# Performance work log

Measured on AMD Instinct MI355X. Metric: run time of the kernel, lower is better.

The kernel has to match this reference:

```python
import jax, jax.numpy as jnp
import numpy as np

NUM_CLASSES = 20
IOU_T = 0.5
NEG_RATIO = 3.0
VXY = 0.1
VWH = 0.2
EPS16 = 9.765625e-4  # torch.finfo(torch.float16).eps


def ltrb2xywh(b):
    return jnp.concatenate([(b[..., :2] + b[..., 2:]) * 0.5, b[..., 2:] - b[..., :2]], -1)


def xywh2ltrb(b):
    return jnp.concatenate([b[..., :2] - b[..., 2:] * 0.5, b[..., :2] + b[..., 2:] * 0.5], -1)


def pairwise_iou(gb, ab):
    # gb [G,4] ltrb, ab [A,4] ltrb -> [G,A]
    lt = jnp.maximum(gb[:, None, :2], ab[None, :, :2])
    rb = jnp.minimum(gb[:, None, 2:], ab[None, :, 2:])
    wh = jnp.clip(rb - lt, 0.0)
    inter = wh[..., 0] * wh[..., 1]
    area_g = (gb[:, 2] - gb[:, 0]) * (gb[:, 3] - gb[:, 1])
    area_a = (ab[:, 2] - ab[:, 0]) * (ab[:, 3] - ab[:, 1])
    return inter / jnp.clip(area_g[:, None] + area_a[None, :] - inter, 1e-8)


def setup_inputs() -> dict:
    key = jax.random.key(0)
    k = jax.random.split(key, 7)
    B, A, G, C = 64, 8732, 50, NUM_CLASSES + 1
    preg = jax.random.normal(k[0], (B, 4, A), jnp.float32) * 0.1
    pcls = jax.random.normal(k[1], (B, C, A), jnp.float32)
    acxy = jax.random.uniform(k[2], (A, 2), jnp.float32)
    awh = jax.random.uniform(k[3], (A, 2), jnp.float32, 0.05, 0.5)
    ancs_xywh = jnp.concatenate([acxy, awh], -1)
    gcxy = jax.random.uniform(k[4], (B, G, 2), jnp.float32, 0.2, 0.8)
    gwh = jax.random.uniform(k[5], (B, G, 2), jnp.float32, 0.05, 0.4)
    gboxes_ltrb = jnp.concatenate([gcxy - gwh * 0.5, gcxy + gwh * 0.5], -1)
    glabels = jax.random.randint(k[6], (B, G), 0, C)  # 0 == padding/background
    return {"preg": preg, "pcls": pcls, "ancs_xywh": ancs_xywh,
            "gboxes_ltrb": gboxes_ltrb, "glabels": glabels}


def _loss(preg, pcls, ancs_xywh, gboxes_ltrb, glabels):
    B, _, A = preg.shape
    preg_bad = jnp.transpose(preg, (0, 2, 1))  # [B,A,4]
    anc_ltrb = xywh2ltrb(ancs_xywh)

    def match(gb, gl):
        iou = pairwise_iou(gb, anc_ltrb)                    # [G,A]
        iou = jnp.where((gl > 0)[:, None], iou, -1.0)       # mask padded gts
        return jnp.argmax(iou, 0), jnp.max(iou, 0) >= IOU_T  # best gt per anchor, pos mask

    boxes_index, mask_pos = jax.vmap(match)(gboxes_ltrb, glabels)  # [B,A],[B,A]

    glabel = jnp.where(mask_pos, jnp.take_along_axis(glabels, boxes_index, 1), 0)  # [B,A]
    gbox_ltrb = jnp.take_along_axis(gboxes_ltrb, boxes_index[..., None], 1)        # [B,A,4]

    gxywh = ltrb2xywh(gbox_ltrb)
    txy = (gxywh[..., :2] - ancs_xywh[None, :, :2]) / (ancs_xywh[None, :, 2:] * VXY)
    twh = jnp.log(jnp.clip(gxywh[..., 2:], 1e-6) / ancs_xywh[None, :, 2:]) / VWH
    gtxywh = jnp.concatenate([txy, twh], -1)
    d = preg_bad - gtxywh
    ad = jnp.abs(d)
    sl1 = jnp.where(ad < 1.0, 0.5 * d * d, ad - 0.5).sum(-1)   # [B,A]
    posf = mask_pos.astype(preg.dtype)
    n_pos_total = jnp.clip(posf.sum(), 1.0)
    l_box = (sl1 * posf).sum() / n_pos_total

    # ---- classification: CE + OHEM hard negatives ----
    logp = jax.nn.log_softmax(pcls, axis=1)                     # [B,C,A]
    ce = -jnp.take_along_axis(logp, glabel[:, None, :], 1)[:, 0, :]  # [B,A]
    nums_pos = jnp.clip(posf.sum(-1), EPS16)                    # [B]

    loss_neg = jnp.where(mask_pos, 0.0, ce)
    order = jnp.argsort(-loss_neg, axis=-1)
    rank = jnp.argsort(order, axis=-1)
    mask_neg = (rank < (NEG_RATIO * nums_pos)[:, None]) & (~mask_pos)
    negf = mask_neg.astype(preg.dtype)

    l_conf_pos = ((ce * posf).sum(-1) / nums_pos).mean()
    l_conf_neg = ((ce * negf).sum(-1) / nums_pos).mean()
    return l_box + l_conf_pos + l_conf_neg


def reference(preg, pcls, ancs_xywh, gboxes_ltrb, glabels):
    return _loss(preg, pcls, ancs_xywh, gboxes_ltrb, glabels)
```

## Files before the change

kernel.cpp:

```cpp
#include <hip/hip_runtime.h>

#define B_ 64
#define A_ 8732
#define G_ 50
#define C_ 21
#define NBA 9
#define NBB 18
#define NV 35

__global__ __launch_bounds__(256) void k_match(
    const float* __restrict__ preg,
    const float* __restrict__ ancs,
    const float* __restrict__ gbox,
    const int*   __restrict__ glab,
    unsigned char* __restrict__ lab_out,
    int*   __restrict__ pos_part,
    float* __restrict__ sl1_part)
{
    __shared__ float4 sg[G_];
    __shared__ float  sa[G_];
    __shared__ int    slb[G_];
    __shared__ float  redf[4];
    __shared__ int    redi[4];
    const int b = blockIdx.y, tid = threadIdx.x;
    const int wid = tid >> 6, lane = tid & 63;
    int a0 = blockIdx.x * 1024 + tid * 4;
    const bool valid = a0 < A_;
    if (!valid) a0 = A_ - 4;

    if (tid < G_) {
        float4 gp = ((const float4*)gbox)[b * G_ + tid];
        const int lb = glab[b * G_ + tid];
        slb[tid] = lb;
        if (lb <= 0) gp = make_float4(1e18f, 1e18f, 1e18f, 1e18f);
        sg[tid] = gp;
        sa[tid] = (gp.z - gp.x) * (gp.w - gp.y);
    }
    __syncthreads();

    float4 apx[4];
    float al[4], at[4], ar[4], ab[4], aa[4];
    #pragma unroll
    for (int j = 0; j < 4; ++j) {
        const float4 ap = ((const float4*)ancs)[a0 + j];
        apx[j] = ap;
        al[j] = ap.x - ap.z * 0.5f; at[j] = ap.y - ap.w * 0.5f;
        ar[j] = ap.x + ap.z * 0.5f; ab[j] = ap.y + ap.w * 0.5f;
        aa[j] = (ar[j] - al[j]) * (ab[j] - at[j]);
    }

    float bin[4] = {-1.f, -1.f, -1.f, -1.f};
    float bun[4] = {1.f, 1.f, 1.f, 1.f};
    int   bgi[4] = {0, 0, 0, 0};
    for (int g = 0; g < G_; ++g) {
        const float4 g4 = sg[g];
        const float  ag = sa[g];
        #pragma unroll
        for (int j = 0; j < 4; ++j) {
            const float ix = fmaxf(fminf(g4.z, ar[j]) - fmaxf(g4.x, al[j]), 0.0f);
            const float iy = fmaxf(fminf(g4.w, ab[j]) - fmaxf(g4.y, at[j]), 0.0f);
            const float in_ = ix * iy;
            const float un  = fmaxf(ag + aa[j] - in_, 1e-8f);
            if (in_ * bun[j] > bin[j] * un) { bin[j] = in_; bun[j] = un; bgi[j] = g; }
        }
    }

    unsigned lbl_pack = 0u;
    float sl1 = 0.0f; int pcnt = 0;
    const float* pr = preg + (size_t)b * 4 * A_ + a0;
    #pragma unroll
    for (int j = 0; j < 4; ++j) {
        const bool pos = valid && (2.0f * bin[j] >= bun[j]);
        const int lab = pos ? slb[bgi[j]] : 0;
        lbl_pack |= ((unsigned)lab) << (8 * j);
        if (pos) {
            const float4 g4 = sg[bgi[j]];
            const float4 ap = apx[j];
            const float gcx = (g4.x + g4.z) * 0.5f, gcy = (g4.y + g4.w) * 0.5f;
            const float t0 = (gcx - ap.x) / (ap.z * 0.1f);
            const float t1 = (gcy - ap.y) / (ap.w * 0.1f);
            const float t2 = __logf(fmaxf(g4.z - g4.x, 1e-6f) / ap.z) * 5.0f;
            const float t3 = __logf(fmaxf(g4.w - g4.y, 1e-6f) / ap.w) * 5.0f;
            #pragma unroll
            for (int k = 0; k < 4; ++k) {
                const float tv = (k == 0) ? t0 : (k == 1) ? t1 : (k == 2) ? t2 : t3;
                const float d  = pr[(size_t)k * A_ + j] - tv;
                const float ad = fabsf(d);
                sl1 += (ad < 1.0f) ? 0.5f * d * d : ad - 0.5f;
            }
            ++pcnt;
        }
    }
    if (valid) *(unsigned*)(lab_out + (size_t)b * A_ + a0) = lbl_pack;

    for (int o = 32; o > 0; o >>= 1) {
        sl1  += __shfl_down(sl1, o);
        pcnt += __shfl_down(pcnt, o);
    }
    if (lane == 0) { redf[wid] = sl1; redi[wid] = pcnt; }
    __syncthreads();
    if (tid == 0) {
        const int slot = b * NBA + blockIdx.x;
        pos_part[slot] = redi[0] + redi[1] + redi[2] + redi[3];
        sl1_part[slot] = redf[0] + redf[1] + redf[2] + redf[3];
    }
}

__global__ __launch_bounds__(256) void k_ce(
    const float* __restrict__ pcls,
    const unsigned char* __restrict__ lab_in,
    float* __restrict__ loss_neg,
    float* __restrict__ cep_part)
{
    __shared__ float redf[4];
    const int b = blockIdx.y, tid = threadIdx.x;
    const int wid = tid >> 6, lane = tid & 63;
    const int pr_i = blockIdx.x * 256 + tid;
    const bool valid = (pr_i * 2) < A_;
    const int a0 = (valid ? pr_i : (A_ / 2 - 1)) * 2;

    const unsigned char* lp = lab_in + (size_t)b * A_ + a0;
    const int lab0 = lp[0], lab1 = lp[1];

    const float* pc = pcls + (size_t)b * C_ * A_ + a0;
    float2 xv[C_];
    #pragma unroll
    for (int c = 0; c < C_; ++c) xv[c] = *(const float2*)(pc + (size_t)c * A_);
    float s0 = 0.0f, s1 = 0.0f, xl0 = 0.0f, xl1 = 0.0f;
    #pragma unroll
    for (int c = 0; c < C_; ++c) {
        s0 += __expf(xv[c].x);
        s1 += __expf(xv[c].y);
        xl0 = (c == lab0) ? xv[c].x : xl0;
        xl1 = (c == lab1) ? xv[c].y : xl1;
    }
    const float ce0 = __logf(s0) - xl0;
    const float ce1 = __logf(s1) - xl1;
    const bool pos0 = lab0 > 0, pos1 = lab1 > 0;

    if (valid)
        *(float2*)(loss_neg + (size_t)b * A_ + a0) =
            make_float2(pos0 ? 0.0f : ce0, pos1 ? 0.0f : ce1);

    float cep = valid ? ((pos0 ? ce0 : 0.0f) + (pos1 ? ce1 : 0.0f)) : 0.0f;
    for (int o = 32; o > 0; o >>= 1) cep += __shfl_down(cep, o);
    if (lane == 0) redf[wid] = cep;
    __syncthreads();
    if (tid == 0)
        cep_part[b * NBB + blockIdx.x] = redf[0] + redf[1] + redf[2] + redf[3];
}

__global__ __launch_bounds__(256) void k_ohem(
    const float* __restrict__ loss_neg,
    const int*   __restrict__ pos_part,
    const float* __restrict__ cep_part,
    float* __restrict__ conf)
{
    __shared__ int   sred[4];
    __shared__ float sredf[4];
    __shared__ int   snp[1];
    const int b = blockIdx.x, tid = threadIdx.x;
    const int wid = tid >> 6, lane = tid & 63;

    unsigned v[NV];
    const float* src = loss_neg + (size_t)b * A_;
    #pragma unroll
    for (int i = 0; i < NV; ++i) {
        const int idx = i * 256 + tid;
        v[i] = (idx < A_) ? __float_as_uint(src[idx]) : 0u;
    }

    unsigned mx = 0u;
    #pragma unroll
    for (int i = 0; i < NV; ++i) mx = max(mx, v[i]);
    for (int o = 32; o > 0; o >>= 1)
        mx = max(mx, (unsigned)__shfl_xor((int)mx, o));
    if (lane == 0) sred[wid] = (int)mx;

    int np_l = 0; float cep_l = 0.0f;
    if (tid < NBA) np_l = pos_part[b * NBA + tid];
    if (tid < NBB) cep_l = cep_part[b * NBB + tid];
    if (wid == 0) {
        for (int o = 32; o > 0; o >>= 1) {
            np_l  += __shfl_xor(np_l, o);
            cep_l += __shfl_xor(cep_l, o);
        }
        if (lane == 0) snp[0] = np_l;
    }
    __syncthreads();
    const unsigned mxall = max(max((unsigned)sred[0], (unsigned)sred[1]),
                               max((unsigned)sred[2], (unsigned)sred[3]));
    const int np = snp[0];
    __syncthreads();

    if (np == 0) {
        if (tid == 0) conf[b] = __uint_as_float(mxall) * 1024.0f * (1.0f / (float)B_);
        return;
    }
    const int K = min(3 * np, A_);

    unsigned thr = 0u;
    for (int bit = 30; bit >= 0; --bit) {
        const unsigned cand = thr | (1u << bit);
        if (cand > mxall) continue;
        int c = 0;
        #pragma unroll
        for (int i = 0; i < NV; ++i)
            c += __builtin_popcountll(__ballot(v[i] >= cand));
        if (lane == 0) sred[wid] = c;
        __syncthreads();
        const int tot = sred[0] + sred[1] + sred[2] + sred[3];
        __syncthreads();
        if (tot >= K) thr = cand;
    }

    float ss = 0.0f; int cgt = 0;
    #pragma unroll
    for (int i = 0; i < NV; ++i) {
        if (v[i] > thr) { ss += __uint_as_float(v[i]); ++cgt; }
    }
    for (int o = 32; o > 0; o >>= 1) {
        ss  += __shfl_xor(ss, o);
        cgt += __shfl_xor(cgt, o);
    }
    if (lane == 0) { sredf[wid] = ss; sred[wid] = cgt; }
    __syncthreads();
    if (tid == 0) {
        const float sgt = sredf[0] + sredf[1] + sredf[2] + sredf[3];
        const int   ngt = sred[0] + sred[1] + sred[2] + sred[3];
        const float t = __uint_as_float(thr);
        const float fnp = (float)np;
        const float l_neg = (sgt + (float)(K - ngt) * t) / fnp;
        const float l_pos = cep_l / fnp;
        conf[b] = (l_neg + l_pos) * (1.0f / (float)B_);
    }
}

__global__ __launch_bounds__(64) void k_final(
    const int*   __restrict__ pos_part,
    const float* __restrict__ sl1_part,
    const float* __restrict__ conf,
    float* __restrict__ out)
{
    const int lane = threadIdx.x;
    int tot = 0; float s1 = 0.0f;
    for (int j = lane; j < B_ * NBA; j += 64) { tot += pos_part[j]; s1 += sl1_part[j]; }
    float cf = conf[lane];
    for (int o = 32; o > 0; o >>= 1) {
        tot += __shfl_xor(tot, o);
        s1  += __shfl_xor(s1, o);
        cf  += __shfl_xor(cf, o);
    }
    if (lane == 0) out[0] = s1 / fmaxf((float)tot, 1.0f) + cf;
}

extern "C" void kernel_launch(void* const* d_in, const int* in_sizes, int n_in,
                              void* d_out, int out_size, void* d_ws, size_t ws_size,
                              hipStream_t stream)
{
    const float* preg = (const float*)d_in[0];
    const float* pcls = (const float*)d_in[1];
    const float* ancs = (const float*)d_in[2];
    const float* gbox = (const float*)d_in[3];
    const int*   glab = (const int*)d_in[4];
    float* out = (float*)d_out;

    float* loss_neg = (float*)d_ws;
    unsigned char* lab_ws = (unsigned char*)(loss_neg + (size_t)B_ * A_);
    int*   pos_part = (int*)(lab_ws + (size_t)B_ * A_);
    float* sl1_part = (float*)(pos_part + B_ * NBA);
    float* cep_part = sl1_part + B_ * NBA;
    float* conf     = cep_part + B_ * NBB;

    dim3 gA(NBA, B_), gB(NBB, B_);
    k_match<<<gA, 256, 0, stream>>>(preg, ancs, gbox, glab, lab_ws, pos_part, sl1_part);
    k_ce<<<gB, 256, 0, stream>>>(pcls, lab_ws, loss_neg, cep_part);
    k_ohem<<<B_, 256, 0, stream>>>(loss_neg, pos_part, cep_part, conf);
    k_final<<<1, 64, 0, stream>>>(pos_part, sl1_part, conf, out);
}
```

Before: 133.9 us.

## Fuse anchor matching and cross-entropy into one kernel

Merges the matching kernel and the softmax cross-entropy kernel into a single kernel, so labels stay in registers and the byte label buffer write and read are removed, along with one launch. Each thread now handles 4 anchors with float4 loads of the class logits, which cuts the CE grid from 18 to 9 blocks per image. It also drops the shared gt-area table in favour of recomputing the area, and removes the union clamp. The risk is lower parallelism for the bandwidth-heavy logit reads (576 blocks total) and more register pressure per thread.

```diff
diff --git a/kernel.cpp b/kernel.cpp
--- a/kernel.cpp
+++ b/kernel.cpp
@@ -4,23 +4,23 @@
 #define A_ 8732
 #define G_ 50
 #define C_ 21
-#define NBA 9
-#define NBB 18
+#define NBF 9
 #define NV 35
 
-__global__ __launch_bounds__(256) void k_match(
+__global__ __launch_bounds__(256) void k_fused(
     const float* __restrict__ preg,
+    const float* __restrict__ pcls,
     const float* __restrict__ ancs,
     const float* __restrict__ gbox,
     const int*   __restrict__ glab,
-    unsigned char* __restrict__ lab_out,
+    float* __restrict__ loss_neg,
     int*   __restrict__ pos_part,
-    float* __restrict__ sl1_part)
+    float* __restrict__ sl1_part,
+    float* __restrict__ cep_part)
 {
     __shared__ float4 sg[G_];
-    __shared__ float  sa[G_];
     __shared__ int    slb[G_];
-    __shared__ float  redf[4];
+    __shared__ float  redf[8];
     __shared__ int    redi[4];
     const int b = blockIdx.y, tid = threadIdx.x;
     const int wid = tid >> 6, lane = tid & 63;
@@ -34,16 +34,13 @@
         slb[tid] = lb;
         if (lb <= 0) gp = make_float4(1e18f, 1e18f, 1e18f, 1e18f);
         sg[tid] = gp;
-        sa[tid] = (gp.z - gp.x) * (gp.w - gp.y);
-    }
-    __syncthreads();
-
-    float4 apx[4];
+    }
+    __syncthreads();
+
     float al[4], at[4], ar[4], ab[4], aa[4];
     #pragma unroll
     for (int j = 0; j < 4; ++j) {
         const float4 ap = ((const float4*)ancs)[a0 + j];
-        apx[j] = ap;
         al[j] = ap.x - ap.z * 0.5f; at[j] = ap.y - ap.w * 0.5f;
         ar[j] = ap.x + ap.z * 0.5f; ab[j] = ap.y + ap.w * 0.5f;
         aa[j] = (ar[j] - al[j]) * (ab[j] - at[j]);
@@ -54,28 +51,52 @@
     int   bgi[4] = {0, 0, 0, 0};
     for (int g = 0; g < G_; ++g) {
         const float4 g4 = sg[g];
-        const float  ag = sa[g];
+        const float  ag = (g4.z - g4.x) * (g4.w - g4.y);
         #pragma unroll
         for (int j = 0; j < 4; ++j) {
             const float ix = fmaxf(fminf(g4.z, ar[j]) - fmaxf(g4.x, al[j]), 0.0f);
             const float iy = fmaxf(fminf(g4.w, ab[j]) - fmaxf(g4.y, at[j]), 0.0f);
             const float in_ = ix * iy;
-            const float un  = fmaxf(ag + aa[j] - in_, 1e-8f);
+            const float un  = ag + aa[j] - in_;
             if (in_ * bun[j] > bin[j] * un) { bin[j] = in_; bun[j] = un; bgi[j] = g; }
         }
     }
 
-    unsigned lbl_pack = 0u;
-    float sl1 = 0.0f; int pcnt = 0;
+    bool pos[4]; int lab[4];
+    #pragma unroll
+    for (int j = 0; j < 4; ++j) {
+        pos[j] = valid && (2.0f * bin[j] >= bun[j]);
+        lab[j] = pos[j] ? slb[bgi[j]] : 0;
+    }
+
+    const float4* pc4 = (const float4*)(pcls + (size_t)b * C_ * A_) + (a0 >> 2);
+    float s[4] = {0.f, 0.f, 0.f, 0.f}, xl[4] = {0.f, 0.f, 0.f, 0.f};
+    #pragma unroll
+    for (int c = 0; c < C_; ++c) {
+        const float4 v = pc4[(size_t)c * (A_ / 4)];
+        s[0] += __expf(v.x); s[1] += __expf(v.y);
+        s[2] += __expf(v.z); s[3] += __expf(v.w);
+        xl[0] = (c == lab[0]) ? v.x : xl[0];
+        xl[1] = (c == lab[1]) ? v.y : xl[1];
+        xl[2] = (c == lab[2]) ? v.z : xl[2];
+        xl[3] = (c == lab[3]) ? v.w : xl[3];
+    }
+    float ce[4];
+    #pragma unroll
+    for (int j = 0; j < 4; ++j) ce[j] = __logf(s[j]) - xl[j];
+
+    if (valid)
+        *(float4*)(loss_neg + (size_t)b * A_ + a0) =
+            make_float4(pos[0] ? 0.f : ce[0], pos[1] ? 0.f : ce[1],
+                        pos[2] ? 0.f : ce[2], pos[3] ? 0.f : ce[3]);
+
+    float sl1 = 0.0f, cep = 0.0f; int pcnt = 0;
     const float* pr = preg + (size_t)b * 4 * A_ + a0;
     #pragma unroll
     for (int j = 0; j < 4; ++j) {
-        const bool pos = valid && (2.0f * bin[j] >= bun[j]);
-        const int lab = pos ? slb[bgi[j]] : 0;
-        lbl_pack |= ((unsigned)lab) << (8 * j);
-        if (pos) {
+        if (pos[j]) {
             const float4 g4 = sg[bgi[j]];
-            const float4 ap = apx[j];
+            const float4 ap = ((const float4*)ancs)[a0 + j];
             const float gcx = (g4.x + g4.z) * 0.5f, gcy = (g4.y + g4.w) * 0.5f;
             const float t0 = (gcx - ap.x) / (ap.z * 0.1f);
             const float t1 = (gcy - ap.y) / (ap.w * 0.1f);
@@ -88,66 +109,23 @@
                 const float ad = fabsf(d);
                 sl1 += (ad < 1.0f) ? 0.5f * d * d : ad - 0.5f;
             }
-            ++pcnt;
+            cep += ce[j]; ++pcnt;
         }
     }
-    if (valid) *(unsigned*)(lab_out + (size_t)b * A_ + a0) = lbl_pack;
 
     for (int o = 32; o > 0; o >>= 1) {
         sl1  += __shfl_down(sl1, o);
+        cep  += __shfl_down(cep, o);
         pcnt += __shfl_down(pcnt, o);
     }
-    if (lane == 0) { redf[wid] = sl1; redi[wid] = pcnt; }
+    if (lane == 0) { redf[wid] = sl1; redf[4 + wid] = cep; redi[wid] = pcnt; }
     __syncthreads();
     if (tid == 0) {
-        const int slot = b * NBA + blockIdx.x;
+        const int slot = b * NBF + blockIdx.x;
         pos_part[slot] = redi[0] + redi[1] + redi[2] + redi[3];
         sl1_part[slot] = redf[0] + redf[1] + redf[2] + redf[3];
-    }
-}
-
-__global__ __launch_bounds__(256) void k_ce(
-    const float* __restrict__ pcls,
-    const unsigned char* __restrict__ lab_in,
-    float* __restrict__ loss_neg,
-    float* __restrict__ cep_part)
-{
-    __shared__ float redf[4];
-    const int b = blockIdx.y, tid = threadIdx.x;
-    const int wid = tid >> 6, lane = tid & 63;
-    const int pr_i = blockIdx.x * 256 + tid;
-    const bool valid = (pr_i * 2) < A_;
-    const int a0 = (valid ? pr_i : (A_ / 2 - 1)) * 2;
-
-    const unsigned char* lp = lab_in + (size_t)b * A_ + a0;
-    const int lab0 = lp[0], lab1 = lp[1];
-
-    const float* pc = pcls + (size_t)b * C_ * A_ + a0;
-    float2 xv[C_];
-    #pragma unroll
-    for (int c = 0; c < C_; ++c) xv[c] = *(const float2*)(pc + (size_t)c * A_);
-    float s0 = 0.0f, s1 = 0.0f, xl0 = 0.0f, xl1 = 0.0f;
-    #pragma unroll
-    for (int c = 0; c < C_; ++c) {
-        s0 += __expf(xv[c].x);
-        s1 += __expf(xv[c].y);
-        xl0 = (c == lab0) ? xv[c].x : xl0;
-        xl1 = (c == lab1) ? xv[c].y : xl1;
-    }
-    const float ce0 = __logf(s0) - xl0;
-    const float ce1 = __logf(s1) - xl1;
-    const bool pos0 = lab0 > 0, pos1 = lab1 > 0;
-
-    if (valid)
-        *(float2*)(loss_neg + (size_t)b * A_ + a0) =
-            make_float2(pos0 ? 0.0f : ce0, pos1 ? 0.0f : ce1);
-
-    float cep = valid ? ((pos0 ? ce0 : 0.0f) + (pos1 ? ce1 : 0.0f)) : 0.0f;
-    for (int o = 32; o > 0; o >>= 1) cep += __shfl_down(cep, o);
-    if (lane == 0) redf[wid] = cep;
-    __syncthreads();
-    if (tid == 0)
-        cep_part[b * NBB + blockIdx.x] = redf[0] + redf[1] + redf[2] + redf[3];
+        cep_part[slot] = redf[4] + redf[5] + redf[6] + redf[7];
+    }
 }
 
 __global__ __launch_bounds__(256) void k_ohem(
@@ -178,8 +156,7 @@
     if (lane == 0) sred[wid] = (int)mx;
 
     int np_l = 0; float cep_l = 0.0f;
-    if (tid < NBA) np_l = pos_part[b * NBA + tid];
-    if (tid < NBB) cep_l = cep_part[b * NBB + tid];
+    if (tid < NBF) { np_l = pos_part[b * NBF + tid]; cep_l = cep_part[b * NBF + tid]; }
     if (wid == 0) {
         for (int o = 32; o > 0; o >>= 1) {
             np_l  += __shfl_xor(np_l, o);
@@ -244,7 +221,7 @@
 {
     const int lane = threadIdx.x;
     int tot = 0; float s1 = 0.0f;
-    for (int j = lane; j < B_ * NBA; j += 64) { tot += pos_part[j]; s1 += sl1_part[j]; }
+    for (int j = lane; j < B_ * NBF; j += 64) { tot += pos_part[j]; s1 += sl1_part[j]; }
     float cf = conf[lane];
     for (int o = 32; o > 0; o >>= 1) {
         tot += __shfl_xor(tot, o);
@@ -266,15 +243,14 @@
     float* out = (float*)d_out;
 
     float* loss_neg = (float*)d_ws;
-    unsigned char* lab_ws = (unsigned char*)(loss_neg + (size_t)B_ * A_);
-    int*   pos_part = (int*)(lab_ws + (size_t)B_ * A_);
-    float* sl1_part = (float*)(pos_part + B_ * NBA);
-    float* cep_part = sl1_part + B_ * NBA;
-    float* conf     = cep_part + B_ * NBB;
-
-    dim3 gA(NBA, B_), gB(NBB, B_);
-    k_match<<<gA, 256, 0, stream>>>(preg, ancs, gbox, glab, lab_ws, pos_part, sl1_part);
-    k_ce<<<gB, 256, 0, stream>>>(pcls, lab_ws, loss_neg, cep_part);
+    int*   pos_part = (int*)(loss_neg + (size_t)B_ * A_);
+    float* sl1_part = (float*)(pos_part + B_ * NBF);
+    float* cep_part = sl1_part + B_ * NBF;
+    float* conf     = cep_part + B_ * NBF;
+
+    dim3 gF(NBF, B_);
+    k_fused<<<gF, 256, 0, stream>>>(preg, pcls, ancs, gbox, glab,
+                                    loss_neg, pos_part, sl1_part, cep_part);
     k_ohem<<<B_, 256, 0, stream>>>(loss_neg, pos_part, cep_part, conf);
     k_final<<<1, 64, 0, stream>>>(pos_part, sl1_part, conf, out);
 }
```

Result: faster. 129.9 us (-3.0%).
